# Kernel tuning notes

Measured on AMD Instinct MI355X. Metric: run time of the kernel, lower is better.

## Reference

```python
import jax, jax.numpy as jnp
import numpy as np
from jax.scipy.special import gammaln, logsumexp

N_SAMPLE, N_GENE, N_TYPE, N_BATCH = 50000, 128, 16, 4


def setup_inputs() -> dict:
    key = jax.random.key(0)
    ks = jax.random.split(key, 7)
    delta = 0.5 * jax.random.normal(ks[0], (N_GENE, N_TYPE), dtype=jnp.float32)
    beta = 0.1 * jax.random.normal(ks[1], (N_BATCH, N_GENE), dtype=jnp.float32)
    # dispersion starts inside the clamp window [1, 100]
    phi = 1.0 + 50.0 * jax.random.uniform(ks[2], (N_GENE,), dtype=jnp.float32)
    # count data (non-negative integers stored as float, as in the torch model)
    expr_mat = jax.random.randint(ks[3], (N_SAMPLE, N_GENE), 0, 20).astype(jnp.float32)
    # design matrix: intercept column + small covariates
    cov = 0.1 * jax.random.uniform(ks[4], (N_SAMPLE, N_BATCH - 1), dtype=jnp.float32)
    cov_mat = jnp.concatenate([jnp.ones((N_SAMPLE, 1), jnp.float32), cov], axis=1)
    # positive size factors around 1
    size_factor = 0.5 + jax.random.uniform(ks[5], (N_SAMPLE,), dtype=jnp.float32)
    marker_onehot = jax.random.randint(ks[6], (N_GENE, N_TYPE), 0, 2).astype(jnp.float32)
    return {"delta": delta, "beta": beta, "phi": phi, "expr_mat": expr_mat,
            "cov_mat": cov_mat, "size_factor": size_factor, "marker_onehot": marker_onehot}


def reference(delta, beta, phi, expr_mat, cov_mat, size_factor, marker_onehot):
    # phi_filter: clamp dispersion to [1, 100]
    phi_f = jnp.clip(phi, 1.0, 100.0)          # [G]
    eta = cov_mat @ beta                        # [S, G] batch effect per gene
    # mu: [S, G, T]
    mu = size_factor[:, None, None] * jnp.exp(eta[:, :, None] + (marker_onehot * delta)[None, :, :])
    phi3 = phi_f[None, :, None]                 # [1, G, 1]
    probs = phi3 / (mu + phi3)                  # NB failure prob param, [S, G, T]
    k = expr_mat[:, :, None]                    # [S, G, 1]
    # nb_logpmf(k, n=phi, p=1-probs) = lgamma(n+k)-lgamma(1+k)-lgamma(n) + k*log(1-probs) + n*log(probs)
    log_pmf = (gammaln(phi3 + k) - gammaln(1.0 + k) - gammaln(phi3)
               + k * jnp.log(1.0 - probs) + phi3 * jnp.log(probs))
    log_probs = log_pmf.sum(axis=1)             # sum over genes -> [S, T]
    log_prob = logsumexp(log_probs, axis=1)     # mixture over cell types -> [S]
    return log_prob.sum()
```

## Files before the change

### kernel.cpp

```cpp
#include <hip/hip_runtime.h>
#include <hip/hip_bf16.h>

#define NG 128
#define NT 16

#define GTAB_OFF 0
#define MDEMD_OFF 1024
#define LGTAB_OFF 5120
#define TAB_FLOATS 7680
#define LN2 0.6931471805599453f
#define L2E 1.4426950408889634f
#define EXP2F(x) __builtin_amdgcn_exp2f(x)

__global__ void setup_kernel(const float* __restrict__ delta,
                             const float* __restrict__ beta,
                             const float* __restrict__ phi,
                             const float* __restrict__ mo,
                             float* __restrict__ ws,
                             float* __restrict__ out) {
    const int g = threadIdx.x;
    if (g == 0) out[0] = 0.0f;
    if (g >= NG) return;

    const float lnfact[20] = {
        0.0f, 0.0f, 0.69314718f, 1.79175947f, 3.17805383f,
        4.78749174f, 6.57925121f, 8.52516132f, 10.60460286f, 12.80182744f,
        15.10441253f, 17.50230781f, 19.98721446f, 22.55216381f, 25.19122114f,
        27.89927134f, 30.67186007f, 33.50507341f, 36.39544517f, 39.33988415f};

    float* gtab  = ws + GTAB_OFF;
    float* mdemd = ws + MDEMD_OFF;
    float* lgtab = ws + LGTAB_OFF;

    float ph = fminf(fmaxf(phi[g], 1.0f), 100.0f);
    float plp = ph * __logf(ph);

    gtab[g * 8 + 0] = beta[0 * NG + g];
    gtab[g * 8 + 1] = beta[1 * NG + g];
    gtab[g * 8 + 2] = beta[2 * NG + g];
    gtab[g * 8 + 3] = beta[3 * NG + g];
    gtab[g * 8 + 4] = ph;
    gtab[g * 8 + 5] = 0.0f;
    gtab[g * 8 + 6] = 0.0f;
    gtab[g * 8 + 7] = 0.0f;

#pragma unroll
    for (int t = 0; t < NT; ++t) {
        float md = mo[g * NT + t] * delta[g * NT + t];
        mdemd[g * 32 + 2 * t]     = md;
        mdemd[g * 32 + 2 * t + 1] = __expf(md);
    }

    float accn = 0.0f;
    lgtab[g * 20 + 0] = plp;
#pragma unroll
    for (int k = 1; k < 20; ++k) {
        accn += __logf(ph + (float)(k - 1));
        lgtab[g * 20 + k] = accn - lnfact[k] + plp;
    }
}

__global__ __launch_bounds__(512) void nb_main(const float* __restrict__ expr,
                                               const float* __restrict__ cov,
                                               const float* __restrict__ sfv,
                                               const float* __restrict__ ws,
                                               float* __restrict__ out,
                                               int ns) {
    __shared__ float s_tab[TAB_FLOATS];

    const int tid = threadIdx.x;
#pragma unroll
    for (int i = 0; i < 4; ++i) {
        int idx = tid + i * 512;
        if (idx < TAB_FLOATS / 4)
            *(float4*)&s_tab[idx * 4] = *(const float4*)(ws + idx * 4);
    }
    __syncthreads();

    const float* __restrict__ s_gt = s_tab + GTAB_OFF;
    const float* __restrict__ s_md = s_tab + MDEMD_OFF;
    const float* __restrict__ s_lg = s_tab + LGTAB_OFF;

    const int lane = tid & 63;
    const int q = __builtin_amdgcn_readfirstlane(tid >> 6);
    const int s = blockIdx.x * 64 + lane;
    const bool valid = (s < ns);

    float acc[NT];
#pragma unroll
    for (int t = 0; t < NT; ++t) acc[t] = 0.0f;
    float hacc = 0.0f;

    float4 cv = make_float4(0.f, 0.f, 0.f, 0.f);
    float sf = 1.0f;
    if (valid) {
        cv = *reinterpret_cast<const float4*>(cov + (size_t)s * 4);
        sf = sfv[s];
    }
    const float lsf  = __logf(sf);
    const float lsf2 = lsf * L2E;

    const int g0 = q * 16;

    for (int g4 = 0; g4 < 4; ++g4) {
        float4 kv = make_float4(0.f, 0.f, 0.f, 0.f);
        if (valid)
            kv = *reinterpret_cast<const float4*>(expr + (size_t)s * NG + g0 + g4 * 4);
        float kfv[4] = {kv.x, kv.y, kv.z, kv.w};
#pragma unroll
        for (int j = 0; j < 4; ++j) {
            const int g = g0 + g4 * 4 + j;
            const float b0 = s_gt[g * 8 + 0];
            const float b1 = s_gt[g * 8 + 1];
            const float b2 = s_gt[g * 8 + 2];
            const float b3 = s_gt[g * 8 + 3];
            const float ph = s_gt[g * 8 + 4];

            float e = fmaf(b3, cv.w, fmaf(b2, cv.z, fmaf(b1, cv.y, b0 * cv.x)));
            float c = EXP2F(fmaf(e, L2E, lsf2));
            float kf = kfv[j];
            float lg = s_lg[g * 20 + (int)kf];
            hacc += fmaf(kf, lsf + e, lg);
            float nkp2 = -(kf + ph) * LN2;
            const float* __restrict__ mp = s_md + g * 32;
#pragma unroll
            for (int t = 0; t < NT; ++t) {
                float md  = mp[2 * t];
                float emd = mp[2 * t + 1];
                float v = fmaf(c, emd, ph);
                acc[t] = fmaf(nkp2, __log2f(v), fmaf(kf, md, acc[t]));
            }
        }
    }
#pragma unroll
    for (int t = 0; t < NT; ++t) acc[t] += hacc;

    float (*red)[64][17] = (float (*)[64][17])s_tab;
    __syncthreads();

    if (q >= 4) {
#pragma unroll
        for (int t = 0; t < NT; ++t) red[q - 4][lane][t] = acc[t];
    }
    __syncthreads();
    if (q < 4) {
#pragma unroll
        for (int t = 0; t < NT; ++t) acc[t] += red[q][lane][t];
    }
    __syncthreads();
    if (q == 2 || q == 3) {
#pragma unroll
        for (int t = 0; t < NT; ++t) red[q - 2][lane][t] = acc[t];
    }
    __syncthreads();
    if (q < 2) {
#pragma unroll
        for (int t = 0; t < NT; ++t) acc[t] += red[q][lane][t];
    }
    __syncthreads();
    if (q == 1) {
#pragma unroll
        for (int t = 0; t < NT; ++t) red[0][lane][t] = acc[t];
    }
    __syncthreads();
    if (q == 0) {
        float m = -1e30f;
#pragma unroll
        for (int t = 0; t < NT; ++t) {
            acc[t] += red[0][lane][t];
            m = fmaxf(m, acc[t]);
        }
        float sum = 0.0f;
#pragma unroll
        for (int t = 0; t < NT; ++t) sum += __expf(acc[t] - m);
        float lp = m + __logf(sum);
        if (!valid) lp = 0.0f;
#pragma unroll
        for (int off = 32; off > 0; off >>= 1) lp += __shfl_down(lp, off);
        if (lane == 0) atomicAdd(out, lp);
    }
}

extern "C" void kernel_launch(void* const* d_in, const int* in_sizes, int n_in,
                              void* d_out, int out_size, void* d_ws, size_t ws_size,
                              hipStream_t stream) {
    const float* delta = (const float*)d_in[0];
    const float* beta  = (const float*)d_in[1];
    const float* phi   = (const float*)d_in[2];
    const float* expr  = (const float*)d_in[3];
    const float* cov   = (const float*)d_in[4];
    const float* sf    = (const float*)d_in[5];
    const float* mo    = (const float*)d_in[6];
    float* out = (float*)d_out;
    float* ws  = (float*)d_ws;
    const int ns = in_sizes[5];

    setup_kernel<<<1, 128, 0, stream>>>(delta, beta, phi, mo, ws, out);

    const int tiles = (ns + 63) / 64;
    nb_main<<<tiles, 512, 0, stream>>>(expr, cov, sf, ws, out, ns);
}
```

Measured before the change: 35.71 us.

## Split gene dimension across four blocks per tile with two-phase reduction

```diff
diff --git a/kernel.cpp b/kernel.cpp
--- a/kernel.cpp
+++ b/kernel.cpp
@@ -5,9 +5,11 @@
 #define NT 16
 
 #define GTAB_OFF 0
-#define MDEMD_OFF 1024
-#define LGTAB_OFF 5120
+#define MD_OFF   1024
+#define EMD_OFF  3072
+#define LG_OFF   5120
 #define TAB_FLOATS 7680
+#define PART_OFF 8192
 #define LN2 0.6931471805599453f
 #define L2E 1.4426950408889634f
 #define EXP2F(x) __builtin_amdgcn_exp2f(x)
@@ -28,63 +30,71 @@
         15.10441253f, 17.50230781f, 19.98721446f, 22.55216381f, 25.19122114f,
         27.89927134f, 30.67186007f, 33.50507341f, 36.39544517f, 39.33988415f};
 
-    float* gtab  = ws + GTAB_OFF;
-    float* mdemd = ws + MDEMD_OFF;
-    float* lgtab = ws + LGTAB_OFF;
-
     float ph = fminf(fmaxf(phi[g], 1.0f), 100.0f);
     float plp = ph * __logf(ph);
 
-    gtab[g * 8 + 0] = beta[0 * NG + g];
-    gtab[g * 8 + 1] = beta[1 * NG + g];
-    gtab[g * 8 + 2] = beta[2 * NG + g];
-    gtab[g * 8 + 3] = beta[3 * NG + g];
-    gtab[g * 8 + 4] = ph;
-    gtab[g * 8 + 5] = 0.0f;
-    gtab[g * 8 + 6] = 0.0f;
-    gtab[g * 8 + 7] = 0.0f;
+    ws[GTAB_OFF + g * 8 + 0] = beta[0 * NG + g];
+    ws[GTAB_OFF + g * 8 + 1] = beta[1 * NG + g];
+    ws[GTAB_OFF + g * 8 + 2] = beta[2 * NG + g];
+    ws[GTAB_OFF + g * 8 + 3] = beta[3 * NG + g];
+    ws[GTAB_OFF + g * 8 + 4] = ph;
+    ws[GTAB_OFF + g * 8 + 5] = 0.0f;
+    ws[GTAB_OFF + g * 8 + 6] = 0.0f;
+    ws[GTAB_OFF + g * 8 + 7] = 0.0f;
 
 #pragma unroll
     for (int t = 0; t < NT; ++t) {
         float md = mo[g * NT + t] * delta[g * NT + t];
-        mdemd[g * 32 + 2 * t]     = md;
-        mdemd[g * 32 + 2 * t + 1] = __expf(md);
+        ws[MD_OFF  + g * 16 + t] = md;
+        ws[EMD_OFF + g * 16 + t] = __expf(md);
     }
 
     float accn = 0.0f;
-    lgtab[g * 20 + 0] = plp;
+    ws[LG_OFF + g * 20 + 0] = plp;
 #pragma unroll
     for (int k = 1; k < 20; ++k) {
         accn += __logf(ph + (float)(k - 1));
-        lgtab[g * 20 + k] = accn - lnfact[k] + plp;
-    }
-}
-
-__global__ __launch_bounds__(512) void nb_main(const float* __restrict__ expr,
-                                               const float* __restrict__ cov,
-                                               const float* __restrict__ sfv,
-                                               const float* __restrict__ ws,
-                                               float* __restrict__ out,
-                                               int ns) {
-    __shared__ float s_tab[TAB_FLOATS];
+        ws[LG_OFF + g * 20 + k] = accn - lnfact[k] + plp;
+    }
+}
+
+__global__ __launch_bounds__(512, 4) void nb_phase1(const float* __restrict__ expr,
+                                                    const float* __restrict__ cov,
+                                                    const float* __restrict__ sfv,
+                                                    const float* __restrict__ ws,
+                                                    float* __restrict__ part_out,
+                                                    int ns, int nsp) {
+    __shared__ float s_tab[4352];
+    float* __restrict__ s_gt  = s_tab;
+    float* __restrict__ s_mdp = s_tab + 256;
+    float* __restrict__ s_emd = s_tab + 768;
+    float* __restrict__ s_lg  = s_tab + 1280;
 
     const int tid = threadIdx.x;
-#pragma unroll
-    for (int i = 0; i < 4; ++i) {
-        int idx = tid + i * 512;
-        if (idx < TAB_FLOATS / 4)
-            *(float4*)&s_tab[idx * 4] = *(const float4*)(ws + idx * 4);
-    }
-    __syncthreads();
-
-    const float* __restrict__ s_gt = s_tab + GTAB_OFF;
-    const float* __restrict__ s_md = s_tab + MDEMD_OFF;
-    const float* __restrict__ s_lg = s_tab + LGTAB_OFF;
+    const int tile = blockIdx.x >> 2;
+    const int quarter = blockIdx.x & 3;
+
+    if (tid < 64)
+        ((float4*)s_gt)[tid] = ((const float4*)(ws + GTAB_OFF + quarter * 256))[tid];
+    else if (tid < 192)
+        ((float4*)s_mdp)[tid - 64] = ((const float4*)(ws + MD_OFF + quarter * 512))[tid - 64];
+    else if (tid < 320)
+        ((float4*)s_emd)[tid - 192] = ((const float4*)(ws + EMD_OFF + quarter * 512))[tid - 192];
+    else if (tid < 480)
+        ((float4*)s_lg)[tid - 320] = ((const float4*)(ws + LG_OFF + quarter * 640))[tid - 320];
+    __syncthreads();
 
     const int lane = tid & 63;
     const int q = __builtin_amdgcn_readfirstlane(tid >> 6);
-    const int s = blockIdx.x * 64 + lane;
+    const int s = tile * 64 + lane;
     const bool valid = (s < ns);
+
+    float emd[4][16];
+#pragma unroll
+    for (int a = 0; a < 4; ++a)
+#pragma unroll
+        for (int t = 0; t < NT; ++t)
+            emd[a][t] = s_emd[(q * 4 + a) * 16 + t];
 
     float acc[NT];
 #pragma unroll
@@ -100,13 +110,158 @@
     const float lsf  = __logf(sf);
     const float lsf2 = lsf * L2E;
 
+    float4 kv = make_float4(0.f, 0.f, 0.f, 0.f);
+    if (valid)
+        kv = *reinterpret_cast<const float4*>(expr + (size_t)s * NG + quarter * 32 + q * 4);
+    float kb[4] = {kv.x, kv.y, kv.z, kv.w};
+
+#pragma unroll
+    for (int a = 0; a < 4; ++a) {
+        const int gl = q * 4 + a;
+        const float b0 = s_gt[gl * 8 + 0];
+        const float b1 = s_gt[gl * 8 + 1];
+        const float b2 = s_gt[gl * 8 + 2];
+        const float b3 = s_gt[gl * 8 + 3];
+        const float ph = s_gt[gl * 8 + 4];
+
+        float e = fmaf(b3, cv.w, fmaf(b2, cv.z, fmaf(b1, cv.y, b0 * cv.x)));
+        float c = EXP2F(fmaf(e, L2E, lsf2));
+        float kf = kb[a];
+        float lg = s_lg[gl * 20 + (int)kf];
+        hacc += fmaf(kf, lsf + e, lg);
+        float nkp2 = -(kf + ph) * LN2;
+#pragma unroll
+        for (int t = 0; t < NT; ++t) {
+            float v = fmaf(c, emd[a][t], ph);
+            acc[t] = fmaf(nkp2, __log2f(v), acc[t]);
+        }
+    }
+
+#pragma unroll
+    for (int a = 0; a < 4; ++a) {
+        const int gl = q * 4 + a;
+        const float kf = kb[a];
+#pragma unroll
+        for (int t = 0; t < NT; ++t)
+            acc[t] = fmaf(kf, s_mdp[gl * 16 + t], acc[t]);
+    }
+#pragma unroll
+    for (int t = 0; t < NT; ++t) acc[t] += hacc;
+
+    __syncthreads();
+    float (*red)[64][17] = (float (*)[64][17])s_tab;
+
+    if (q >= 4) {
+#pragma unroll
+        for (int t = 0; t < NT; ++t) red[q - 4][lane][t] = acc[t];
+    }
+    __syncthreads();
+    if (q < 4) {
+#pragma unroll
+        for (int t = 0; t < NT; ++t) acc[t] += red[q][lane][t];
+    }
+    __syncthreads();
+    if (q == 2 || q == 3) {
+#pragma unroll
+        for (int t = 0; t < NT; ++t) red[q - 2][lane][t] = acc[t];
+    }
+    __syncthreads();
+    if (q < 2) {
+#pragma unroll
+        for (int t = 0; t < NT; ++t) acc[t] += red[q][lane][t];
+    }
+    __syncthreads();
+    if (q == 1) {
+#pragma unroll
+        for (int t = 0; t < NT; ++t) red[0][lane][t] = acc[t];
+    }
+    __syncthreads();
+    if (q == 0) {
+#pragma unroll
+        for (int t = 0; t < NT; ++t) {
+            float v = acc[t] + red[0][lane][t];
+            part_out[(size_t)(quarter * NT + t) * nsp + tile * 64 + lane] = v;
+        }
+    }
+}
+
+__global__ __launch_bounds__(256) void nb_phase2(const float* __restrict__ part_in,
+                                                 float* __restrict__ out,
+                                                 int ns, int nsp) {
+    const int s = blockIdx.x * 256 + threadIdx.x;
+    float lp = 0.0f;
+    if (s < ns) {
+        float tot[NT];
+#pragma unroll
+        for (int t = 0; t < NT; ++t) tot[t] = 0.0f;
+#pragma unroll
+        for (int qt = 0; qt < 4; ++qt) {
+#pragma unroll
+            for (int t = 0; t < NT; ++t)
+                tot[t] += part_in[(size_t)(qt * NT + t) * nsp + s];
+        }
+        float m = tot[0];
+#pragma unroll
+        for (int t = 1; t < NT; ++t) m = fmaxf(m, tot[t]);
+        float sum = 0.0f;
+#pragma unroll
+        for (int t = 0; t < NT; ++t) sum += __expf(tot[t] - m);
+        lp = m + __logf(sum);
+    }
+#pragma unroll
+    for (int off = 32; off > 0; off >>= 1) lp += __shfl_down(lp, off);
+    __shared__ float r[4];
+    if ((threadIdx.x & 63) == 0) r[threadIdx.x >> 6] = lp;
+    __syncthreads();
+    if (threadIdx.x == 0) atomicAdd(out, r[0] + r[1] + r[2] + r[3]);
+}
+
+__global__ __launch_bounds__(512) void nb_single(const float* __restrict__ expr,
+                                                 const float* __restrict__ cov,
+                                                 const float* __restrict__ sfv,
+                                                 const float* __restrict__ ws,
+                                                 float* __restrict__ out,
+                                                 int ns) {
+    __shared__ float s_tab[TAB_FLOATS];
+    const int tid = threadIdx.x;
+#pragma unroll
+    for (int i = 0; i < 4; ++i) {
+        int idx = tid + i * 512;
+        if (idx < TAB_FLOATS / 4)
+            *(float4*)&s_tab[idx * 4] = *(const float4*)(ws + idx * 4);
+    }
+    __syncthreads();
+
+    const float* __restrict__ s_gt  = s_tab + GTAB_OFF;
+    const float* __restrict__ s_mdp = s_tab + MD_OFF;
+    const float* __restrict__ s_emd = s_tab + EMD_OFF;
+    const float* __restrict__ s_lg  = s_tab + LG_OFF;
+
+    const int lane = tid & 63;
+    const int q = __builtin_amdgcn_readfirstlane(tid >> 6);
+    const int s = blockIdx.x * 64 + lane;
+    const bool valid = (s < ns);
+
+    float acc[NT];
+#pragma unroll
+    for (int t = 0; t < NT; ++t) acc[t] = 0.0f;
+    float hacc = 0.0f;
+
+    float4 cv = make_float4(0.f, 0.f, 0.f, 0.f);
+    float sf = 1.0f;
+    if (valid) {
+        cv = *reinterpret_cast<const float4*>(cov + (size_t)s * 4);
+        sf = sfv[s];
+    }
+    const float lsf  = __logf(sf);
+    const float lsf2 = lsf * L2E;
     const int g0 = q * 16;
 
     for (int g4 = 0; g4 < 4; ++g4) {
-        float4 kv = make_float4(0.f, 0.f, 0.f, 0.f);
+        float4 kvv = make_float4(0.f, 0.f, 0.f, 0.f);
         if (valid)
-            kv = *reinterpret_cast<const float4*>(expr + (size_t)s * NG + g0 + g4 * 4);
-        float kfv[4] = {kv.x, kv.y, kv.z, kv.w};
+            kvv = *reinterpret_cast<const float4*>(expr + (size_t)s * NG + g0 + g4 * 4);
+        float kfv[4] = {kvv.x, kvv.y, kvv.z, kvv.w};
 #pragma unroll
         for (int j = 0; j < 4; ++j) {
             const int g = g0 + g4 * 4 + j;
@@ -122,13 +277,10 @@
             float lg = s_lg[g * 20 + (int)kf];
             hacc += fmaf(kf, lsf + e, lg);
             float nkp2 = -(kf + ph) * LN2;
-            const float* __restrict__ mp = s_md + g * 32;
 #pragma unroll
             for (int t = 0; t < NT; ++t) {
-                float md  = mp[2 * t];
-                float emd = mp[2 * t + 1];
-                float v = fmaf(c, emd, ph);
-                acc[t] = fmaf(nkp2, __log2f(v), fmaf(kf, md, acc[t]));
+                float v = fmaf(c, s_emd[g * 16 + t], ph);
+                acc[t] = fmaf(nkp2, __log2f(v), fmaf(kf, s_mdp[g * 16 + t], acc[t]));
             }
         }
     }
@@ -137,7 +289,6 @@
 
     float (*red)[64][17] = (float (*)[64][17])s_tab;
     __syncthreads();
-
     if (q >= 4) {
 #pragma unroll
         for (int t = 0; t < NT; ++t) red[q - 4][lane][t] = acc[t];
@@ -198,5 +349,14 @@
     setup_kernel<<<1, 128, 0, stream>>>(delta, beta, phi, mo, ws, out);
 
     const int tiles = (ns + 63) / 64;
-    nb_main<<<tiles, 512, 0, stream>>>(expr, cov, sf, ws, out, ns);
-}
+    const int nsp = tiles * 64;
+    const size_t need = ((size_t)PART_OFF + 64ull * (size_t)nsp) * 4ull;
+
+    if (ws_size >= need) {
+        float* part = ws + PART_OFF;
+        nb_phase1<<<tiles * 4, 512, 0, stream>>>(expr, cov, sf, ws, part, ns, nsp);
+        nb_phase2<<<(ns + 255) / 256, 256, 0, stream>>>(part, out, ns, nsp);
+    } else {
+        nb_single<<<tiles, 512, 0, stream>>>(expr, cov, sf, ws, out, ns);
+    }
+}
```

Measured after the change: 51.74 us. 1.45x slower.
